# Performance work log

Hardware: AMD Instinct MI355X
Metric: run time of the kernel (lower is better)

The kernel has to match this reference:

```python
import jax, jax.numpy as jnp
import numpy as np

B, S, D, DQKV = 4, 2048, 1024, 1024

def setup_inputs() -> dict:
    key = jax.random.key(0)
    kx, kq, kk, kv = jax.random.split(key, 4)
    scale = 1.0 / np.sqrt(D)
    return {
        "x": jax.random.normal(kx, (B, S, D), dtype=jnp.float32),
        "wq": jax.random.normal(kq, (D, DQKV), dtype=jnp.float32) * scale,
        "wk": jax.random.normal(kk, (D, DQKV), dtype=jnp.float32) * scale,
        "wv": jax.random.normal(kv, (D, DQKV), dtype=jnp.float32) * scale,
    }

def reference(x, wq, wk, wv):
    # QKV projections: [B,S,D] @ [D,Dqkv] -> [B,S,Dqkv]
    q = jnp.einsum('bsd,de->bse', x, wq)
    k = jnp.einsum('bsd,de->bse', x, wk)
    v = jnp.einsum('bsd,de->bse', x, wv)
    # scores: [B,S,S], scaled by sqrt(dim_qkv)
    scores = jnp.einsum('bik,bjk->bij', q, k) / jnp.sqrt(jnp.asarray(DQKV, dtype=x.dtype))
    attn = jax.nn.softmax(scores, axis=-1)
    # output: [B,S,Dqkv]
    return jnp.einsum('bij,bjd->bid', attn, v)
```

## Files before the change

kernel.cpp:

```cpp
#include <hip/hip_runtime.h>
#include <cstdint>
#include <cstddef>

typedef __bf16 bf16;
typedef __bf16 bf16x4 __attribute__((ext_vector_type(4)));
typedef __bf16 bf16x8 __attribute__((ext_vector_type(8)));
typedef float  f32x4  __attribute__((ext_vector_type(4)));

#define BATCH 4
#define SEQ   2048
#define DIM   1024
#define LDP   2112

__device__ __forceinline__ bf16 to_bf16(float f) {
    unsigned u = __builtin_bit_cast(unsigned, f);
    u += 0x7fffu + ((u >> 16) & 1u);
    unsigned short h = (unsigned short)(u >> 16);
    return __builtin_bit_cast(bf16, h);
}

__device__ __forceinline__ void load16_lds(const bf16* g, bf16* l) {
    __builtin_amdgcn_global_load_lds(
        (__attribute__((address_space(1))) void*)(g),
        (__attribute__((address_space(3))) void*)(l),
        16, 0, 0);
}

#define BARRIER() __builtin_amdgcn_s_barrier()
#define LGKM0()   asm volatile("s_waitcnt lgkmcnt(0)")
#define VM0()     asm volatile("s_waitcnt vmcnt(0)")
#define VM3()     asm volatile("s_waitcnt vmcnt(3)")
#define VM4()     asm volatile("s_waitcnt vmcnt(4)")


__device__ __forceinline__ void stage_r32(
    const bf16* __restrict__ srcRow0, int ld, int k0, bf16* dstBase)
{
    const int t = threadIdx.x;
    const int r = t >> 2;
    const int c = (t & 3) ^ ((r >> 1) & 3);
    load16_lds(srcRow0 + (size_t)r * ld + k0 + c * 8,
               dstBase + (t >> 6) * 512);
}

__device__ __forceinline__ void gemm_p3w_core(
    const bf16* __restrict__ Ablk, const bf16* __restrict__ Bblk,
    int K, int lda, int ldb, bf16* As, bf16* Bs, f32x4 acc[8][4])
{
    const int tid  = threadIdx.x;
    const int lane = tid & 63;
    const int wave = tid >> 6;
    const int wr   = wave >> 2;
    const int wc   = wave & 3;
    const int r16  = lane & 15;
    const int g    = lane >> 4;
    const int NT   = K >> 5;
    const int arow0 = wr * 128 + r16;
    const int brow0 = wc * 64 + r16;

    stage_r32(Ablk, lda, 0, As);
    stage_r32(Ablk + (size_t)128 * lda, lda, 0, As + 4096);
    stage_r32(Bblk, ldb, 0, Bs);
    stage_r32(Bblk + (size_t)128 * ldb, ldb, 0, Bs + 4096);
    stage_r32(Ablk, lda, 32, As + 8192);
    stage_r32(Ablk + (size_t)128 * lda, lda, 32, As + 8192 + 4096);
    stage_r32(Bblk, ldb, 32, Bs + 8192);
    stage_r32(Bblk + (size_t)128 * ldb, ldb, 32, Bs + 8192 + 4096);
    VM4();
    BARRIER();

    int c0 = 0, c2 = 2;
    for (int t = 0; t < NT; ++t) {
        bf16* Ac = As + c0 * 8192;
        bf16* Bc = Bs + c0 * 8192;

        bf16x8 a[8], b[4];
#pragma unroll
        for (int n = 0; n < 4; ++n) {
            const int R = brow0 + n * 16;
            b[n] = *(const bf16x8*)(Bc + R * 32 + ((g ^ ((R >> 1) & 3)) * 8));
        }
#pragma unroll
        for (int m = 0; m < 8; ++m) {
            const int R = arow0 + m * 16;
            a[m] = *(const bf16x8*)(Ac + R * 32 + ((g ^ ((R >> 1) & 3)) * 8));
        }
        if (t + 2 < NT) {
            const int k2 = (t + 2) << 5;
            bf16* An = As + c2 * 8192;
            bf16* Bn = Bs + c2 * 8192;
            stage_r32(Ablk, lda, k2, An);
            stage_r32(Ablk + (size_t)128 * lda, lda, k2, An + 4096);
            stage_r32(Bblk, ldb, k2, Bn);
            stage_r32(Bblk + (size_t)128 * ldb, ldb, k2, Bn + 4096);
        }
        __builtin_amdgcn_s_setprio(1);
#pragma unroll
        for (int m = 0; m < 8; ++m)
#pragma unroll
            for (int n = 0; n < 4; ++n)
                acc[m][n] = __builtin_amdgcn_mfma_f32_16x16x32_bf16(
                    a[m], b[n], acc[m][n], 0, 0, 0);
        __builtin_amdgcn_s_setprio(0);

        LGKM0();
        if (t + 1 < NT) {
            if (t + 2 < NT) { VM4(); } else { VM0(); }
        }
        BARRIER();
        c0 = (c0 == 2) ? 0 : c0 + 1;
        c2 = (c2 == 2) ? 0 : c2 + 1;
    }
}

__device__ __forceinline__ void gemm_p3s_core(
    const bf16* __restrict__ Ablk, const bf16* __restrict__ Bblk,
    int K, int lda, int ldb, bf16* As, bf16* Bs, f32x4 acc[4][4])
{
    const int tid  = threadIdx.x;
    const int lane = tid & 63;
    const int wave = tid >> 6;
    const int wr   = wave >> 1;
    const int wc   = wave & 1;
    const int r16  = lane & 15;
    const int g    = lane >> 4;
    const int NT   = K >> 5;
    const int arow0 = wr * 64 + r16;
    const int brow0 = wc * 64 + r16;

    stage_r32(Ablk, lda, 0, As);
    stage_r32(Ablk + (size_t)128 * lda, lda, 0, As + 4096);
    stage_r32(Bblk, ldb, 0, Bs);
    stage_r32(Ablk, lda, 32, As + 8192);
    stage_r32(Ablk + (size_t)128 * lda, lda, 32, As + 8192 + 4096);
    stage_r32(Bblk, ldb, 32, Bs + 4096);
    VM3();
    BARRIER();

    int c0 = 0, c2 = 2;
    for (int t = 0; t < NT; ++t) {
        bf16* Ac = As + c0 * 8192;
        bf16* Bc = Bs + c0 * 4096;

        bf16x8 a[4], b[4];
#pragma unroll
        for (int n = 0; n < 4; ++n) {
            const int R = brow0 + n * 16;
            b[n] = *(const bf16x8*)(Bc + R * 32 + ((g ^ ((R >> 1) & 3)) * 8));
        }
#pragma unroll
        for (int m = 0; m < 4; ++m) {
            const int R = arow0 + m * 16;
            a[m] = *(const bf16x8*)(Ac + R * 32 + ((g ^ ((R >> 1) & 3)) * 8));
        }
        if (t + 2 < NT) {
            const int k2 = (t + 2) << 5;
            bf16* An = As + c2 * 8192;
            bf16* Bn = Bs + c2 * 4096;
            stage_r32(Ablk, lda, k2, An);
            stage_r32(Ablk + (size_t)128 * lda, lda, k2, An + 4096);
            stage_r32(Bblk, ldb, k2, Bn);
        }
        __builtin_amdgcn_s_setprio(1);
#pragma unroll
        for (int m = 0; m < 4; ++m)
#pragma unroll
            for (int n = 0; n < 4; ++n)
                acc[m][n] = __builtin_amdgcn_mfma_f32_16x16x32_bf16(
                    a[m], b[n], acc[m][n], 0, 0, 0);
        __builtin_amdgcn_s_setprio(0);

        LGKM0();
        if (t + 1 < NT) {
            if (t + 2 < NT) { VM3(); } else { VM0(); }
        }
        BARRIER();
        c0 = (c0 == 2) ? 0 : c0 + 1;
        c2 = (c2 == 2) ? 0 : c2 + 1;
    }
}

__device__ __forceinline__ void write_c256w(
    bf16* __restrict__ Cb, int ldc, const f32x4 acc[8][4])
{
    const int lane = threadIdx.x & 63;
    const int wave = threadIdx.x >> 6;
    const int wr = wave >> 2, wc = wave & 3;
    const int r16 = lane & 15, g = lane >> 4;
    const int row0 = wr * 128 + g * 4;
    const int col0 = wc * 64 + r16;
#pragma unroll
    for (int m = 0; m < 8; ++m)
#pragma unroll
        for (int n = 0; n < 4; ++n)
#pragma unroll
            for (int rr = 0; rr < 4; ++rr)
                Cb[(size_t)(row0 + m * 16 + rr) * ldc + col0 + n * 16] =
                    to_bf16(acc[m][n][rr]);
}

__device__ __forceinline__ void write_c128s(
    bf16* __restrict__ Cb, int ldc, const f32x4 acc[4][4])
{
    const int lane = threadIdx.x & 63;
    const int wave = threadIdx.x >> 6;
    const int wr = wave >> 1, wc = wave & 1;
    const int r16 = lane & 15, g = lane >> 4;
    const int row0 = wr * 64 + g * 4;
    const int col0 = wc * 64 + r16;
#pragma unroll
    for (int m = 0; m < 4; ++m)
#pragma unroll
        for (int n = 0; n < 4; ++n)
#pragma unroll
            for (int rr = 0; rr < 4; ++rr)
                Cb[(size_t)(row0 + m * 16 + rr) * ldc + col0 + n * 16] =
                    to_bf16(acc[m][n][rr]);
}

__global__ __launch_bounds__(512, 2) void proj_qk_w(
    const bf16* __restrict__ xb, const bf16* __restrict__ Wt,
    bf16* __restrict__ Q, bf16* __restrict__ Kb)
{
    __shared__ bf16 As[24576];
    __shared__ bf16 Bs[24576];
    f32x4 acc[8][4] = {};

    const int p = blockIdx.x;
    const int x = p & 7, s = p >> 3;
    const int my = x * 4 + (s >> 3);
    const int j  = s & 7;
    const bf16* Ab = xb + (size_t)my * 256 * DIM;
    const bf16* Bb = Wt + (size_t)((j >> 2) ? DIM * DIM : 0)
                        + (size_t)(j & 3) * 256 * DIM;
    bf16* dst = (j >> 2) ? Kb : Q;
    bf16* Cb = dst + (size_t)my * 256 * DIM + (size_t)(j & 3) * 256;

    gemm_p3w_core(Ab, Bb, DIM, DIM, DIM, As, Bs, acc);
    write_c256w(Cb, DIM, acc);
}

__global__ __launch_bounds__(512, 2) void proj_v_s(
    const bf16* __restrict__ xb, const bf16* __restrict__ Wt,
    bf16* __restrict__ Vt)
{
    __shared__ bf16 As[24576];
    __shared__ bf16 Bs[12288];
    f32x4 acc[4][4] = {};

    const int p = blockIdx.x;
    const int x = p & 7, s = p >> 3;
    const int bz = x & 3;
    const int vx = (x >> 2) * 8 + (s & 7);
    const int vy = s >> 3;
    const bf16* Ab = Wt + (size_t)2 * DIM * DIM + (size_t)vy * 256 * DIM;
    const bf16* Bb = xb + (size_t)bz * SEQ * DIM + (size_t)vx * 128 * DIM;
    bf16* Cb = Vt + (size_t)bz * DIM * LDP + (size_t)vy * 256 * LDP
                  + (size_t)vx * 128;

    gemm_p3s_core(Ab, Bb, DIM, DIM, DIM, As, Bs, acc);
    write_c128s(Cb, LDP, acc);
}

__global__ __launch_bounds__(512, 2) void gemm_scores_w(
    const bf16* __restrict__ Qm, const bf16* __restrict__ Kb,
    bf16* __restrict__ P, float* __restrict__ lsumP)
{
    __shared__ bf16 As[24576];
    __shared__ bf16 Bs[24576];
    __shared__ float rbuf[256][4];
    f32x4 acc[8][4] = {};

    const int p = blockIdx.x;
    const int x = p & 7, s = p >> 3;
    const int bz = x & 3;
    const int by = (x >> 2) * 4 + (s >> 3);
    const int bxg = s & 7;
    const bf16* Ab = Qm + (size_t)bz * SEQ * DIM + (size_t)by * 256 * DIM;
    const bf16* Bb = Kb + (size_t)bz * SEQ * DIM + (size_t)bxg * 256 * DIM;
    gemm_p3w_core(Ab, Bb, DIM, DIM, DIM, As, Bs, acc);

    bf16* Cb = P + (size_t)bz * SEQ * LDP;
    const int lane = threadIdx.x & 63;
    const int wave = threadIdx.x >> 6;
    const int wr = wave >> 2, wc = wave & 3;
    const int r16 = lane & 15, g = lane >> 4;
    const int rowL0 = wr * 128 + g * 4;
    const int colB  = bxg * 256 + wc * 64 + r16;
#pragma unroll
    for (int m = 0; m < 8; ++m)
#pragma unroll
        for (int rr = 0; rr < 4; ++rr) {
            float sum = 0.0f;
#pragma unroll
            for (int n = 0; n < 4; ++n) {
                const float e = __expf(acc[m][n][rr] * 0.03125f);
                sum += e;
                Cb[(size_t)(by * 256 + rowL0 + m * 16 + rr) * LDP
                   + colB + n * 16] = to_bf16(e);
            }
            sum += __shfl_xor(sum, 1);
            sum += __shfl_xor(sum, 2);
            sum += __shfl_xor(sum, 4);
            sum += __shfl_xor(sum, 8);
            if (r16 == 0)
                rbuf[rowL0 + m * 16 + rr][wc] = sum;
        }
    BARRIER();
    if (threadIdx.x < 256) {
        const int r = threadIdx.x;
        const float tot = rbuf[r][0] + rbuf[r][1] + rbuf[r][2] + rbuf[r][3];
        lsumP[((size_t)bz * 8 + bxg) * SEQ + by * 256 + r] = tot;
    }
}

__global__ __launch_bounds__(512, 2) void gemm_pv_s(
    const bf16* __restrict__ P, const bf16* __restrict__ Vt,
    float* __restrict__ C, const float* __restrict__ lsumP)
{
    __shared__ bf16 As[24576];
    __shared__ bf16 Bs[12288];
    __shared__ float sbuf[256];
    f32x4 acc[4][4] = {};

    const int p = blockIdx.x;
    const int x = p & 7, s = p >> 3;
    const int bz = x & 3;
    const int by = (x >> 2) * 4 + (s >> 3);
    const int bx = s & 7;
    const bf16* Ab = P  + (size_t)bz * SEQ * LDP + (size_t)by * 256 * LDP;
    const bf16* Bb = Vt + (size_t)bz * DIM * LDP + (size_t)bx * 128 * LDP;
    gemm_p3s_core(Ab, Bb, SEQ, LDP, LDP, As, Bs, acc);

    if (threadIdx.x < 256) {
        const int r = threadIdx.x;
        const size_t base = (size_t)bz * 8 * SEQ + by * 256 + r;
        float t = 0.0f;
#pragma unroll
        for (int jj = 0; jj < 8; ++jj)
            t += lsumP[base + (size_t)jj * SEQ];
        sbuf[r] = t;
    }
    BARRIER();

    float* Cb = C + (size_t)bz * SEQ * DIM;
    const int lane = threadIdx.x & 63;
    const int wave = threadIdx.x >> 6;
    const int wr = wave >> 1, wc = wave & 1;
    const int r16 = lane & 15, g = lane >> 4;
    const int rowL0 = wr * 64 + g * 4;
    const int col0  = bx * 128 + wc * 64 + r16;
#pragma unroll
    for (int m = 0; m < 4; ++m)
#pragma unroll
        for (int rr = 0; rr < 4; ++rr) {
            const int rl = rowL0 + m * 16 + rr;
            const float inv = __builtin_amdgcn_rcpf(sbuf[rl]);
            const int row = by * 256 + rl;
#pragma unroll
            for (int n = 0; n < 4; ++n)
                Cb[(size_t)row * DIM + col0 + n * 16] = acc[m][n][rr] * inv;
        }
}

__global__ __launch_bounds__(256) void prep(
    const float* __restrict__ x,  const float* __restrict__ wq,
    const float* __restrict__ wk, const float* __restrict__ wv,
    bf16* __restrict__ xb, bf16* __restrict__ Wt)
{
    __shared__ float tile[32][33];
    const int b = blockIdx.x;
    const int tid = threadIdx.x;
    if (b < 8192) {
        const size_t i = ((size_t)b * 256 + tid) * 4;
        const float4 v = *(const float4*)(x + i);
        bf16x4 o = { to_bf16(v.x), to_bf16(v.y), to_bf16(v.z), to_bf16(v.w) };
        *(bf16x4*)(xb + i) = o;
    } else {
        const int t   = b - 8192;
        const int sel = t >> 10;
        const int n0  = (t & 31) * 32;
        const int k0  = ((t >> 5) & 31) * 32;
        const float* w = (sel == 0) ? wq : (sel == 1) ? wk : wv;
        const int tx = tid & 31, ty = tid >> 5;
#pragma unroll
        for (int j = 0; j < 32; j += 8)
            tile[ty + j][tx] = w[(size_t)(k0 + ty + j) * 1024 + n0 + tx];
        __syncthreads();
        bf16* dst = Wt + (size_t)sel * 1024 * 1024;
#pragma unroll
        for (int j = 0; j < 32; j += 8)
            dst[(size_t)(n0 + ty + j) * 1024 + k0 + tx] = to_bf16(tile[tx][ty + j]);
    }
}

extern "C" void kernel_launch(void* const* d_in, const int* in_sizes, int n_in,
                              void* d_out, int out_size, void* d_ws, size_t ws_size,
                              hipStream_t stream)
{
    const float* x  = (const float*)d_in[0];
    const float* wq = (const float*)d_in[1];
    const float* wk = (const float*)d_in[2];
    const float* wv = (const float*)d_in[3];
    float* out = (float*)d_out;
    char* ws = (char*)d_ws;

    bf16*  xb    = (bf16*)(ws);
    bf16*  Wt    = (bf16*)(ws + (16u << 20));
    bf16*  Q     = (bf16*)(ws + (22u << 20));
    bf16*  Kb    = (bf16*)(ws + (38u << 20));
    bf16*  Vt    = (bf16*)(ws + (54u << 20));
    bf16*  P     = (bf16*)(ws + (72u << 20));
    float* lsumP = (float*)(ws + (108u << 20));

    prep<<<dim3(8192 + 3072), dim3(256), 0, stream>>>(
        x, wq, wk, wv, xb, Wt);

    proj_qk_w<<<dim3(256), dim3(512), 0, stream>>>(xb, Wt, Q, Kb);
    proj_v_s<<<dim3(256), dim3(512), 0, stream>>>(xb, Wt, Vt);

    gemm_scores_w<<<dim3(256), dim3(512), 0, stream>>>(Q, Kb, P, lsumP);

    gemm_pv_s<<<dim3(256), dim3(512), 0, stream>>>(P, Vt, out, lsumP);
}
```

Measured before the change: 226.0 us.

## Fuse all attention stages into one cooperative kernel with grid syncs

```diff
diff --git a/kernel.cpp b/kernel.cpp
--- a/kernel.cpp
+++ b/kernel.cpp
@@ -1,6 +1,9 @@
 #include <hip/hip_runtime.h>
+#include <hip/hip_cooperative_groups.h>
 #include <cstdint>
 #include <cstddef>
+
+namespace cg = cooperative_groups;
 
 typedef __bf16 bf16;
 typedef __bf16 bf16x4 __attribute__((ext_vector_type(4)));
@@ -218,179 +221,166 @@
                     to_bf16(acc[m][n][rr]);
 }
 
-__global__ __launch_bounds__(512, 2) void proj_qk_w(
-    const bf16* __restrict__ xb, const bf16* __restrict__ Wt,
-    bf16* __restrict__ Q, bf16* __restrict__ Kb)
-{
-    __shared__ bf16 As[24576];
-    __shared__ bf16 Bs[24576];
-    f32x4 acc[8][4] = {};
-
-    const int p = blockIdx.x;
-    const int x = p & 7, s = p >> 3;
-    const int my = x * 4 + (s >> 3);
-    const int j  = s & 7;
-    const bf16* Ab = xb + (size_t)my * 256 * DIM;
-    const bf16* Bb = Wt + (size_t)((j >> 2) ? DIM * DIM : 0)
-                        + (size_t)(j & 3) * 256 * DIM;
-    bf16* dst = (j >> 2) ? Kb : Q;
-    bf16* Cb = dst + (size_t)my * 256 * DIM + (size_t)(j & 3) * 256;
-
-    gemm_p3w_core(Ab, Bb, DIM, DIM, DIM, As, Bs, acc);
-    write_c256w(Cb, DIM, acc);
-}
-
-__global__ __launch_bounds__(512, 2) void proj_v_s(
-    const bf16* __restrict__ xb, const bf16* __restrict__ Wt,
-    bf16* __restrict__ Vt)
-{
-    __shared__ bf16 As[24576];
-    __shared__ bf16 Bs[12288];
-    f32x4 acc[4][4] = {};
-
-    const int p = blockIdx.x;
-    const int x = p & 7, s = p >> 3;
-    const int bz = x & 3;
-    const int vx = (x >> 2) * 8 + (s & 7);
-    const int vy = s >> 3;
-    const bf16* Ab = Wt + (size_t)2 * DIM * DIM + (size_t)vy * 256 * DIM;
-    const bf16* Bb = xb + (size_t)bz * SEQ * DIM + (size_t)vx * 128 * DIM;
-    bf16* Cb = Vt + (size_t)bz * DIM * LDP + (size_t)vy * 256 * LDP
-                  + (size_t)vx * 128;
-
-    gemm_p3s_core(Ab, Bb, DIM, DIM, DIM, As, Bs, acc);
-    write_c128s(Cb, LDP, acc);
-}
-
-__global__ __launch_bounds__(512, 2) void gemm_scores_w(
-    const bf16* __restrict__ Qm, const bf16* __restrict__ Kb,
-    bf16* __restrict__ P, float* __restrict__ lsumP)
-{
+__global__ __launch_bounds__(512, 2) void fused_attn(
+    const float* __restrict__ x,  const float* __restrict__ wq,
+    const float* __restrict__ wk, const float* __restrict__ wv,
+    bf16* __restrict__ xb, bf16* __restrict__ Wt,
+    bf16* __restrict__ Q,  bf16* __restrict__ Kb, bf16* __restrict__ Vt,
+    bf16* __restrict__ P,  float* __restrict__ lsumP,
+    float* __restrict__ out)
+{
+    cg::grid_group grid = cg::this_grid();
     __shared__ bf16 As[24576];
     __shared__ bf16 Bs[24576];
     __shared__ float rbuf[256][4];
-    f32x4 acc[8][4] = {};
-
-    const int p = blockIdx.x;
-    const int x = p & 7, s = p >> 3;
-    const int bz = x & 3;
-    const int by = (x >> 2) * 4 + (s >> 3);
-    const int bxg = s & 7;
-    const bf16* Ab = Qm + (size_t)bz * SEQ * DIM + (size_t)by * 256 * DIM;
-    const bf16* Bb = Kb + (size_t)bz * SEQ * DIM + (size_t)bxg * 256 * DIM;
-    gemm_p3w_core(Ab, Bb, DIM, DIM, DIM, As, Bs, acc);
-
-    bf16* Cb = P + (size_t)bz * SEQ * LDP;
-    const int lane = threadIdx.x & 63;
-    const int wave = threadIdx.x >> 6;
-    const int wr = wave >> 2, wc = wave & 3;
-    const int r16 = lane & 15, g = lane >> 4;
-    const int rowL0 = wr * 128 + g * 4;
-    const int colB  = bxg * 256 + wc * 64 + r16;
-#pragma unroll
-    for (int m = 0; m < 8; ++m)
-#pragma unroll
-        for (int rr = 0; rr < 4; ++rr) {
-            float sum = 0.0f;
-#pragma unroll
-            for (int n = 0; n < 4; ++n) {
-                const float e = __expf(acc[m][n][rr] * 0.03125f);
-                sum += e;
-                Cb[(size_t)(by * 256 + rowL0 + m * 16 + rr) * LDP
-                   + colB + n * 16] = to_bf16(e);
+    __shared__ float sbuf[256];
+
+    const int p   = blockIdx.x;
+    const int tid = threadIdx.x;
+    const int xq  = p & 7, s = p >> 3;
+
+    {
+        const float4* x4 = (const float4*)x;
+#pragma unroll 4
+        for (int i = 0; i < 16; ++i) {
+            const size_t idx = (size_t)i * 131072 + (size_t)p * 512 + tid;
+            const float4 v = x4[idx];
+            bf16x4 o = { to_bf16(v.x), to_bf16(v.y), to_bf16(v.z), to_bf16(v.w) };
+            *(bf16x4*)(xb + idx * 4) = o;
+        }
+        float (*tb)[32][33] = (float(*)[32][33])As;
+        const int ts = tid >> 8;
+        const int tl = tid & 255;
+        const int tx = tl & 31, ty = tl >> 5;
+        for (int ii = 0; ii < 6; ++ii) {
+            const int tile = p * 12 + ii * 2 + ts;
+            const int sel = tile >> 10, rem = tile & 1023;
+            const int n0 = (rem & 31) * 32, k0 = (rem >> 5) * 32;
+            const float* w = (sel == 0) ? wq : (sel == 1) ? wk : wv;
+#pragma unroll
+            for (int j = 0; j < 32; j += 8)
+                tb[ts][ty + j][tx] = w[(size_t)(k0 + ty + j) * 1024 + n0 + tx];
+            __syncthreads();
+            bf16* dst = Wt + (size_t)sel * 1024 * 1024;
+#pragma unroll
+            for (int j = 0; j < 32; j += 8)
+                dst[(size_t)(n0 + ty + j) * 1024 + k0 + tx] =
+                    to_bf16(tb[ts][tx][ty + j]);
+            __syncthreads();
+        }
+    }
+    grid.sync();
+
+    {
+        f32x4 acc[8][4] = {};
+        const int my = xq * 4 + (s >> 3);
+        const int j  = s & 7;
+        const bf16* Ab = xb + (size_t)my * 256 * DIM;
+        const bf16* Bb = Wt + (size_t)((j >> 2) ? DIM * DIM : 0)
+                            + (size_t)(j & 3) * 256 * DIM;
+        bf16* dst = (j >> 2) ? Kb : Q;
+        bf16* Cb = dst + (size_t)my * 256 * DIM + (size_t)(j & 3) * 256;
+        gemm_p3w_core(Ab, Bb, DIM, DIM, DIM, As, Bs, acc);
+        write_c256w(Cb, DIM, acc);
+    }
+    grid.sync();
+
+    {
+        f32x4 acc[4][4] = {};
+        const int bz = xq & 3;
+        const int vx = (xq >> 2) * 8 + (s & 7);
+        const int vy = s >> 3;
+        const bf16* Ab = Wt + (size_t)2 * DIM * DIM + (size_t)vy * 256 * DIM;
+        const bf16* Bb = xb + (size_t)bz * SEQ * DIM + (size_t)vx * 128 * DIM;
+        bf16* Cb = Vt + (size_t)bz * DIM * LDP + (size_t)vy * 256 * LDP
+                      + (size_t)vx * 128;
+        gemm_p3s_core(Ab, Bb, DIM, DIM, DIM, As, Bs, acc);
+        write_c128s(Cb, LDP, acc);
+    }
+    grid.sync();
+
+    {
+        f32x4 acc[8][4] = {};
+        const int bz = xq & 3;
+        const int by = (xq >> 2) * 4 + (s >> 3);
+        const int bxg = s & 7;
+        const bf16* Ab = Q  + (size_t)bz * SEQ * DIM + (size_t)by * 256 * DIM;
+        const bf16* Bb = Kb + (size_t)bz * SEQ * DIM + (size_t)bxg * 256 * DIM;
+        gemm_p3w_core(Ab, Bb, DIM, DIM, DIM, As, Bs, acc);
+
+        bf16* Cb = P + (size_t)bz * SEQ * LDP;
+        const int lane = tid & 63;
+        const int wave = tid >> 6;
+        const int wr = wave >> 2, wc = wave & 3;
+        const int r16 = lane & 15, g = lane >> 4;
+        const int rowL0 = wr * 128 + g * 4;
+        const int colB  = bxg * 256 + wc * 64 + r16;
+#pragma unroll
+        for (int m = 0; m < 8; ++m)
+#pragma unroll
+            for (int rr = 0; rr < 4; ++rr) {
+                float sum = 0.0f;
+#pragma unroll
+                for (int n = 0; n < 4; ++n) {
+                    const float e = __expf(acc[m][n][rr] * 0.03125f);
+                    sum += e;
+                    Cb[(size_t)(by * 256 + rowL0 + m * 16 + rr) * LDP
+                       + colB + n * 16] = to_bf16(e);
+                }
+                sum += __shfl_xor(sum, 1);
+                sum += __shfl_xor(sum, 2);
+                sum += __shfl_xor(sum, 4);
+                sum += __shfl_xor(sum, 8);
+                if (r16 == 0)
+                    rbuf[rowL0 + m * 16 + rr][wc] = sum;
             }
-            sum += __shfl_xor(sum, 1);
-            sum += __shfl_xor(sum, 2);
-            sum += __shfl_xor(sum, 4);
-            sum += __shfl_xor(sum, 8);
-            if (r16 == 0)
-                rbuf[rowL0 + m * 16 + rr][wc] = sum;
-        }
-    BARRIER();
-    if (threadIdx.x < 256) {
-        const int r = threadIdx.x;
-        const float tot = rbuf[r][0] + rbuf[r][1] + rbuf[r][2] + rbuf[r][3];
-        lsumP[((size_t)bz * 8 + bxg) * SEQ + by * 256 + r] = tot;
-    }
-}
-
-__global__ __launch_bounds__(512, 2) void gemm_pv_s(
-    const bf16* __restrict__ P, const bf16* __restrict__ Vt,
-    float* __restrict__ C, const float* __restrict__ lsumP)
-{
-    __shared__ bf16 As[24576];
-    __shared__ bf16 Bs[12288];
-    __shared__ float sbuf[256];
-    f32x4 acc[4][4] = {};
-
-    const int p = blockIdx.x;
-    const int x = p & 7, s = p >> 3;
-    const int bz = x & 3;
-    const int by = (x >> 2) * 4 + (s >> 3);
-    const int bx = s & 7;
-    const bf16* Ab = P  + (size_t)bz * SEQ * LDP + (size_t)by * 256 * LDP;
-    const bf16* Bb = Vt + (size_t)bz * DIM * LDP + (size_t)bx * 128 * LDP;
-    gemm_p3s_core(Ab, Bb, SEQ, LDP, LDP, As, Bs, acc);
-
-    if (threadIdx.x < 256) {
-        const int r = threadIdx.x;
-        const size_t base = (size_t)bz * 8 * SEQ + by * 256 + r;
-        float t = 0.0f;
-#pragma unroll
-        for (int jj = 0; jj < 8; ++jj)
-            t += lsumP[base + (size_t)jj * SEQ];
-        sbuf[r] = t;
-    }
-    BARRIER();
-
-    float* Cb = C + (size_t)bz * SEQ * DIM;
-    const int lane = threadIdx.x & 63;
-    const int wave = threadIdx.x >> 6;
-    const int wr = wave >> 1, wc = wave & 1;
-    const int r16 = lane & 15, g = lane >> 4;
-    const int rowL0 = wr * 64 + g * 4;
-    const int col0  = bx * 128 + wc * 64 + r16;
-#pragma unroll
-    for (int m = 0; m < 4; ++m)
-#pragma unroll
-        for (int rr = 0; rr < 4; ++rr) {
-            const int rl = rowL0 + m * 16 + rr;
-            const float inv = __builtin_amdgcn_rcpf(sbuf[rl]);
-            const int row = by * 256 + rl;
-#pragma unroll
-            for (int n = 0; n < 4; ++n)
-                Cb[(size_t)row * DIM + col0 + n * 16] = acc[m][n][rr] * inv;
-        }
-}
-
-__global__ __launch_bounds__(256) void prep(
-    const float* __restrict__ x,  const float* __restrict__ wq,
-    const float* __restrict__ wk, const float* __restrict__ wv,
-    bf16* __restrict__ xb, bf16* __restrict__ Wt)
-{
-    __shared__ float tile[32][33];
-    const int b = blockIdx.x;
-    const int tid = threadIdx.x;
-    if (b < 8192) {
-        const size_t i = ((size_t)b * 256 + tid) * 4;
-        const float4 v = *(const float4*)(x + i);
-        bf16x4 o = { to_bf16(v.x), to_bf16(v.y), to_bf16(v.z), to_bf16(v.w) };
-        *(bf16x4*)(xb + i) = o;
-    } else {
-        const int t   = b - 8192;
-        const int sel = t >> 10;
-        const int n0  = (t & 31) * 32;
-        const int k0  = ((t >> 5) & 31) * 32;
-        const float* w = (sel == 0) ? wq : (sel == 1) ? wk : wv;
-        const int tx = tid & 31, ty = tid >> 5;
-#pragma unroll
-        for (int j = 0; j < 32; j += 8)
-            tile[ty + j][tx] = w[(size_t)(k0 + ty + j) * 1024 + n0 + tx];
-        __syncthreads();
-        bf16* dst = Wt + (size_t)sel * 1024 * 1024;
-#pragma unroll
-        for (int j = 0; j < 32; j += 8)
-            dst[(size_t)(n0 + ty + j) * 1024 + k0 + tx] = to_bf16(tile[tx][ty + j]);
+        BARRIER();
+        if (tid < 256) {
+            const float tot = rbuf[tid][0] + rbuf[tid][1]
+                            + rbuf[tid][2] + rbuf[tid][3];
+            lsumP[((size_t)bz * 8 + bxg) * SEQ + by * 256 + tid] = tot;
+        }
+    }
+    grid.sync();
+
+    {
+        f32x4 acc[4][4] = {};
+        const int bz = xq & 3;
+        const int by = (xq >> 2) * 4 + (s >> 3);
+        const int bx = s & 7;
+        const bf16* Ab = P  + (size_t)bz * SEQ * LDP + (size_t)by * 256 * LDP;
+        const bf16* Bb = Vt + (size_t)bz * DIM * LDP + (size_t)bx * 128 * LDP;
+        gemm_p3s_core(Ab, Bb, SEQ, LDP, LDP, As, Bs, acc);
+
+        if (tid < 256) {
+            const size_t base = (size_t)bz * 8 * SEQ + by * 256 + tid;
+            float t = 0.0f;
+#pragma unroll
+            for (int jj = 0; jj < 8; ++jj)
+                t += lsumP[base + (size_t)jj * SEQ];
+            sbuf[tid] = t;
+        }
+        BARRIER();
+
+        float* Cb = out + (size_t)bz * SEQ * DIM;
+        const int lane = tid & 63;
+        const int wave = tid >> 6;
+        const int wr = wave >> 1, wc = wave & 1;
+        const int r16 = lane & 15, g = lane >> 4;
+        const int rowL0 = wr * 64 + g * 4;
+        const int col0  = bx * 128 + wc * 64 + r16;
+#pragma unroll
+        for (int m = 0; m < 4; ++m)
+#pragma unroll
+            for (int rr = 0; rr < 4; ++rr) {
+                const int rl = rowL0 + m * 16 + rr;
+                const float inv = __builtin_amdgcn_rcpf(sbuf[rl]);
+                const int row = by * 256 + rl;
+#pragma unroll
+                for (int n = 0; n < 4; ++n)
+                    Cb[(size_t)row * DIM + col0 + n * 16] =
+                        acc[m][n][rr] * inv;
+            }
     }
 }
 
@@ -413,13 +403,9 @@
     bf16*  P     = (bf16*)(ws + (72u << 20));
     float* lsumP = (float*)(ws + (108u << 20));
 
-    prep<<<dim3(8192 + 3072), dim3(256), 0, stream>>>(
-        x, wq, wk, wv, xb, Wt);
-
-    proj_qk_w<<<dim3(256), dim3(512), 0, stream>>>(xb, Wt, Q, Kb);
-    proj_v_s<<<dim3(256), dim3(512), 0, stream>>>(xb, Wt, Vt);
-
-    gemm_scores_w<<<dim3(256), dim3(512), 0, stream>>>(Q, Kb, P, lsumP);
-
-    gemm_pv_s<<<dim3(256), dim3(512), 0, stream>>>(P, Vt, out, lsumP);
-}
+    void* args[] = { (void*)&x, (void*)&wq, (void*)&wk, (void*)&wv,
+                     (void*)&xb, (void*)&Wt, (void*)&Q, (void*)&Kb,
+                     (void*)&Vt, (void*)&P, (void*)&lsumP, (void*)&out };
+    hipLaunchCooperativeKernel((const void*)fused_attn,
+                               dim3(256), dim3(512), args, 0, stream);
+}
```

Result: slower. 361.2 us (+59.8%).
